# Performance work log

Measured on AMD Instinct MI355X. Metric: run time of the kernel, lower is better.

The kernel has to match this reference:

```python
import jax, jax.numpy as jnp
import numpy as np

L, B, D = 1024, 128, 256  # max_seq_len, batch (dialogues), modality feature dim


def _lin_init(key, shape, fan_in):
    s = 1.0 / np.sqrt(fan_in)
    return jax.random.uniform(key, shape, jnp.float32, -s, s)


def setup_inputs() -> dict:
    key = jax.random.key(0)
    ks = jax.random.split(key, 12)
    inp = {
        'a': jax.random.normal(ks[0], (L, B, D), jnp.float32),
        'v': jax.random.normal(ks[1], (L, B, D), jnp.float32),
        'l': jax.random.normal(ks[2], (L, B, D), jnp.float32),
        # all dialogues padded to full length -> fixed node count (jit-friendly)
        'lengths': jnp.full((B,), L, dtype=jnp.int32),
        # modality transforms: Linear(mem_dim, cand_dim)
        'Wa': _lin_init(ks[3], (D, D), D), 'ba': jnp.zeros((D,), jnp.float32),
        'Wv': _lin_init(ks[4], (D, D), D), 'bv': jnp.zeros((D,), jnp.float32),
        'Wl': _lin_init(ks[5], (D, D), D), 'bl': jnp.zeros((D,), jnp.float32),
        # pairwise gates: Linear(3*mem_dim, 1)
        'Wav': _lin_init(ks[6], (1, 3 * D), 3 * D), 'bav': jnp.zeros((1,), jnp.float32),
        'Wal': _lin_init(ks[7], (1, 3 * D), 3 * D), 'bal': jnp.zeros((1,), jnp.float32),
        'Wvl': _lin_init(ks[8], (1, 3 * D), 3 * D), 'bvl': jnp.zeros((1,), jnp.float32),
    }
    return inp


def _graphify(x, lengths):
    # simple_batch_graphify: cat_j x[:lengths[j], j, :].  With lengths == L this is
    # exactly the batch-major flattening of the padded tensor (node order preserved).
    return jnp.transpose(x, (1, 0, 2)).reshape(-1, x.shape[-1])  # (B*L, D)


def reference(a, v, l, lengths, Wa, ba, Wv, bv, Wl, bl, Wav, bav, Wal, bal, Wvl, bvl):
    na = _graphify(a, lengths)  # (N, D)
    nv = _graphify(v, lengths)
    nl = _graphify(l, lengths)

    # MMGatedAttention, att_type='general', modals='avl' (dropout = eval identity)
    ha = jnp.tanh(na @ Wa.T + ba)
    hv = jnp.tanh(nv @ Wv.T + bv)
    hl = jnp.tanh(nl @ Wl.T + bl)

    z_av = jax.nn.sigmoid(jnp.concatenate([na, nv, na * nv], axis=-1) @ Wav.T + bav)  # (N,1)
    h_av = z_av * ha + (1.0 - z_av) * hv

    z_al = jax.nn.sigmoid(jnp.concatenate([na, nl, na * nl], axis=-1) @ Wal.T + bal)
    h_al = z_al * ha + (1.0 - z_al) * hl

    z_vl = jax.nn.sigmoid(jnp.concatenate([nv, nl, nv * nl], axis=-1) @ Wvl.T + bvl)
    h_vl = z_vl * hv + (1.0 - z_vl) * hl

    return jnp.concatenate([h_av, h_al, h_vl], axis=-1)  # (N, 3D)
```

## Files before the change

kernel.cpp:

```cpp
#include <hip/hip_runtime.h>
#include <hip/hip_bf16.h>

#define L_SEQ 1024
#define B_DLG 128
#define D_DIM 256
#define BM 32
#define THREADS 512
#define KSTEPS 8
#define NTILES (L_SEQ / BM)

typedef __attribute__((ext_vector_type(8))) short short8;
typedef __attribute__((ext_vector_type(4))) float f32x4;

__device__ __forceinline__ float bfbits_to_f(unsigned short u) {
    return __uint_as_float(((unsigned int)u) << 16);
}
__device__ __forceinline__ unsigned short f_to_bfbits(float f) {
    unsigned int u = __float_as_uint(f);
    unsigned int r = (u + 0x7FFFu + ((u >> 16) & 1u)) >> 16;
    return (unsigned short)r;
}
__device__ __forceinline__ float fast_tanh(float x) {
    return 1.0f - 2.0f / (__expf(2.0f * x) + 1.0f);
}
__device__ __forceinline__ float fast_sigmoid(float x) {
    return 1.0f / (1.0f + __expf(-x));
}
__device__ __forceinline__ float dot4(float4 x, float4 w) {
    return x.x * w.x + x.y * w.y + x.z * w.z + x.w * w.w;
}

__global__ void wconv_kernel(const float* __restrict__ wa,
                             const float* __restrict__ wv,
                             const float* __restrict__ wl,
                             unsigned short* __restrict__ wb) {
    int i = blockIdx.x * blockDim.x + threadIdx.x;
    int mod  = i >> 13;
    int r    = i & 8191;
    int col  = r >> 5;
    int ks   = (r >> 2) & 7;
    int kblk = r & 3;
    const float* src = (mod == 0) ? wa : (mod == 1) ? wv : wl;
    const float4* s = (const float4*)(src + col * 256 + ks * 32 + kblk * 8);
    float4 lo = s[0], hi = s[1];
    short8 pk;
    pk[0] = (short)f_to_bfbits(lo.x); pk[1] = (short)f_to_bfbits(lo.y);
    pk[2] = (short)f_to_bfbits(lo.z); pk[3] = (short)f_to_bfbits(lo.w);
    pk[4] = (short)f_to_bfbits(hi.x); pk[5] = (short)f_to_bfbits(hi.y);
    pk[6] = (short)f_to_bfbits(hi.z); pk[7] = (short)f_to_bfbits(hi.w);
    int dst = mod * 8192 + (((col >> 4) * 8 + ks) << 6) + kblk * 16 + (col & 15);
    *(short8*)(wb + dst * 8) = pk;
}

__global__ __launch_bounds__(THREADS, 4)
void fused_kernel(const float* __restrict__ a,
                  const float* __restrict__ v,
                  const float* __restrict__ l,
                  const unsigned short* __restrict__ wbf,
                  const float* __restrict__ ba,
                  const float* __restrict__ bv,
                  const float* __restrict__ bl,
                  const float* __restrict__ wav, const float* __restrict__ bav,
                  const float* __restrict__ wal, const float* __restrict__ bal,
                  const float* __restrict__ wvl, const float* __restrict__ bvl,
                  float* __restrict__ out) {
    __shared__ __align__(16) unsigned short lds_a[3][BM][D_DIM];
    __shared__ float lds_z[3][BM];

    const int tid  = threadIdx.x;
    const int wave = tid >> 6;
    const int lane = tid & 63;
    const int bidx = blockIdx.x;
    const int b    = bidx >> 5;
    const int t0   = (bidx & (NTILES - 1)) * BM;

    float4 fa[4], fv[4], fl[4];
#pragma unroll
    for (int i = 0; i < BM / 8; ++i) {
        const int row = wave + 8 * i;
        const size_t gbase = ((size_t)(t0 + row) * B_DLG + b) * D_DIM + lane * 4;
        fa[i] = *(const float4*)(a + gbase);
        fv[i] = *(const float4*)(v + gbase);
        fl[i] = *(const float4*)(l + gbase);
    }

    const int k0 = lane * 4;
    float4 gav0 = *(const float4*)(wav + k0);
    float4 gav1 = *(const float4*)(wav + 256 + k0);
    float4 gav2 = *(const float4*)(wav + 512 + k0);
    float4 gal0 = *(const float4*)(wal + k0);
    float4 gal1 = *(const float4*)(wal + 256 + k0);
    float4 gal2 = *(const float4*)(wal + 512 + k0);
    float4 gvl0 = *(const float4*)(wvl + k0);
    float4 gvl1 = *(const float4*)(wvl + 256 + k0);
    float4 gvl2 = *(const float4*)(wvl + 512 + k0);

    {
        const int swz = (wave & 7) << 4;
        const int boff = (lane * 8) ^ swz;
#pragma unroll
        for (int i = 0; i < BM / 8; ++i) {
            const int row = wave + 8 * i;
            ushort4 pa, pv, pl;
            pa.x = f_to_bfbits(fa[i].x); pa.y = f_to_bfbits(fa[i].y);
            pa.z = f_to_bfbits(fa[i].z); pa.w = f_to_bfbits(fa[i].w);
            pv.x = f_to_bfbits(fv[i].x); pv.y = f_to_bfbits(fv[i].y);
            pv.z = f_to_bfbits(fv[i].z); pv.w = f_to_bfbits(fv[i].w);
            pl.x = f_to_bfbits(fl[i].x); pl.y = f_to_bfbits(fl[i].y);
            pl.z = f_to_bfbits(fl[i].z); pl.w = f_to_bfbits(fl[i].w);
            *(ushort4*)((char*)&lds_a[0][row][0] + boff) = pa;
            *(ushort4*)((char*)&lds_a[1][row][0] + boff) = pv;
            *(ushort4*)((char*)&lds_a[2][row][0] + boff) = pl;

            float4 pav, pal, pvl;
            pav.x = fa[i].x * fv[i].x; pav.y = fa[i].y * fv[i].y;
            pav.z = fa[i].z * fv[i].z; pav.w = fa[i].w * fv[i].w;
            pal.x = fa[i].x * fl[i].x; pal.y = fa[i].y * fl[i].y;
            pal.z = fa[i].z * fl[i].z; pal.w = fa[i].w * fl[i].w;
            pvl.x = fv[i].x * fl[i].x; pvl.y = fv[i].y * fl[i].y;
            pvl.z = fv[i].z * fl[i].z; pvl.w = fv[i].w * fl[i].w;
            float s_av = dot4(fa[i], gav0) + dot4(fv[i], gav1) + dot4(pav, gav2);
            float s_al = dot4(fa[i], gal0) + dot4(fl[i], gal1) + dot4(pal, gal2);
            float s_vl = dot4(fv[i], gvl0) + dot4(fl[i], gvl1) + dot4(pvl, gvl2);

#pragma unroll
            for (int off = 1; off < 64; off <<= 1) {
                s_av += __shfl_xor(s_av, off);
                s_al += __shfl_xor(s_al, off);
                s_vl += __shfl_xor(s_vl, off);
            }
            if (lane == 0) {
                lds_z[0][row] = fast_sigmoid(s_av + bav[0]);
                lds_z[1][row] = fast_sigmoid(s_al + bal[0]);
                lds_z[2][row] = fast_sigmoid(s_vl + bvl[0]);
            }
        }
    }
    __syncthreads();

    f32x4 acc[3][2][2];
#pragma unroll
    for (int m = 0; m < 3; ++m)
#pragma unroll
        for (int mt = 0; mt < 2; ++mt)
#pragma unroll
            for (int ct = 0; ct < 2; ++ct)
                acc[m][mt][ct] = (f32x4){0.f, 0.f, 0.f, 0.f};

    const int l15 = lane & 15;
    const int kblk = lane >> 4;

#pragma unroll 2
    for (int ks = 0; ks < KSTEPS; ++ks) {
        int kbyte = ks * 64 + kblk * 16;
#pragma unroll
        for (int mod = 0; mod < 3; ++mod) {
            short8 afrag[2];
#pragma unroll
            for (int mt = 0; mt < 2; ++mt) {
                int row = mt * 16 + l15;
                int bo = kbyte ^ ((row & 7) << 4);
                afrag[mt] = *(const short8*)((const char*)&lds_a[mod][row][0] + bo);
            }
#pragma unroll
            for (int ct = 0; ct < 2; ++ct) {
                const unsigned short* bp = wbf +
                    ((size_t)(((mod * 16 + wave * 2 + ct) * 8 + ks) * 64) + lane) * 8;
                short8 bfrag = *(const short8*)bp;
#pragma unroll
                for (int mt = 0; mt < 2; ++mt)
                    acc[mod][mt][ct] = __builtin_amdgcn_mfma_f32_16x16x32_bf16(
                        afrag[mt], bfrag, acc[mod][mt][ct], 0, 0, 0);
            }
        }
    }

    __syncthreads();

    const size_t rowbase = (size_t)b * L_SEQ + t0;
    const int colbase = wave * 32;
#pragma unroll
    for (int mt = 0; mt < 2; ++mt) {
#pragma unroll
        for (int ct = 0; ct < 2; ++ct) {
            int col = colbase + ct * 16 + l15;
            float bba = ba[col], bbv = bv[col], bbl = bl[col];
#pragma unroll
            for (int r = 0; r < 4; ++r) {
                int rl_ = mt * 16 + (lane >> 4) * 4 + r;
                float ta = fast_tanh(acc[0][mt][ct][r] + bba);
                float tv = fast_tanh(acc[1][mt][ct][r] + bbv);
                float tl = fast_tanh(acc[2][mt][ct][r] + bbl);
                float zav = lds_z[0][rl_];
                float zal = lds_z[1][rl_];
                float zvl = lds_z[2][rl_];
                float* orow = out + (rowbase + rl_) * (3 * D_DIM);
                orow[col]             = zav * ta + (1.f - zav) * tv;
                orow[D_DIM + col]     = zal * ta + (1.f - zal) * tl;
                orow[2 * D_DIM + col] = zvl * tv + (1.f - zvl) * tl;
            }
        }
    }
}

extern "C" void kernel_launch(void* const* d_in, const int* in_sizes, int n_in,
                              void* d_out, int out_size, void* d_ws, size_t ws_size,
                              hipStream_t stream) {
    const float* a   = (const float*)d_in[0];
    const float* v   = (const float*)d_in[1];
    const float* l   = (const float*)d_in[2];
    const float* Wa  = (const float*)d_in[4];
    const float* ba  = (const float*)d_in[5];
    const float* Wv  = (const float*)d_in[6];
    const float* bv  = (const float*)d_in[7];
    const float* Wl  = (const float*)d_in[8];
    const float* bl  = (const float*)d_in[9];
    const float* Wav = (const float*)d_in[10];
    const float* bav = (const float*)d_in[11];
    const float* Wal = (const float*)d_in[12];
    const float* bal = (const float*)d_in[13];
    const float* Wvl = (const float*)d_in[14];
    const float* bvl = (const float*)d_in[15];
    float* out = (float*)d_out;

    unsigned short* wb = (unsigned short*)d_ws;

    hipLaunchKernelGGL(wconv_kernel, dim3(96), dim3(256), 0, stream, Wa, Wv, Wl, wb);
    hipLaunchKernelGGL(fused_kernel, dim3(B_DLG * NTILES), dim3(THREADS), 0, stream,
                       a, v, l, wb, ba, bv, bl, Wav, bav, Wal, bal, Wvl, bvl, out);
}
```

Measured before the change: 282.6 us.

## Make fused kernel persistent over eight row tiles with register prefetch of next tile

Each block now handles eight consecutive 32-row tiles of one dialogue instead of one, which cuts the grid from 4096 to 512 blocks. Gate weights are staged once into LDS and bias values are hoisted out of the loop. The next tile's a/v/l rows are loaded into registers before the MFMA and epilogue of the current tile, so global-load latency overlaps with compute. In exchange there are fewer blocks to spread across CUs (512 blocks of 512 threads), a serial per-block loop, and extra LDS plus register pressure.

```diff
diff --git a/kernel.cpp b/kernel.cpp
--- a/kernel.cpp
+++ b/kernel.cpp
@@ -7,14 +7,12 @@
 #define BM 32
 #define THREADS 512
 #define KSTEPS 8
-#define NTILES (L_SEQ / BM)
+#define TPB 8
+#define NBLK (B_DLG * (L_SEQ / BM) / TPB)
 
 typedef __attribute__((ext_vector_type(8))) short short8;
 typedef __attribute__((ext_vector_type(4))) float f32x4;
 
-__device__ __forceinline__ float bfbits_to_f(unsigned short u) {
-    return __uint_as_float(((unsigned int)u) << 16);
-}
 __device__ __forceinline__ unsigned short f_to_bfbits(float f) {
     unsigned int u = __float_as_uint(f);
     unsigned int r = (u + 0x7FFFu + ((u >> 16) & 1u)) >> 16;
@@ -65,139 +63,170 @@
                   const float* __restrict__ wvl, const float* __restrict__ bvl,
                   float* __restrict__ out) {
     __shared__ __align__(16) unsigned short lds_a[3][BM][D_DIM];
+    __shared__ __align__(16) float lds_gw[3][3 * D_DIM];
     __shared__ float lds_z[3][BM];
 
     const int tid  = threadIdx.x;
     const int wave = tid >> 6;
     const int lane = tid & 63;
-    const int bidx = blockIdx.x;
-    const int b    = bidx >> 5;
-    const int t0   = (bidx & (NTILES - 1)) * BM;
-
-    float4 fa[4], fv[4], fl[4];
-#pragma unroll
-    for (int i = 0; i < BM / 8; ++i) {
-        const int row = wave + 8 * i;
-        const size_t gbase = ((size_t)(t0 + row) * B_DLG + b) * D_DIM + lane * 4;
-        fa[i] = *(const float4*)(a + gbase);
-        fv[i] = *(const float4*)(v + gbase);
-        fl[i] = *(const float4*)(l + gbase);
+    const int b    = blockIdx.x >> 2;
+    const int t00  = (blockIdx.x & 3) * (TPB * BM);
+
+    for (int i = tid; i < 3 * 3 * D_DIM; i += THREADS) {
+        int g = i / (3 * D_DIM);
+        int k = i - g * (3 * D_DIM);
+        const float* gw = (g == 0) ? wav : (g == 1) ? wal : wvl;
+        lds_gw[g][k] = gw[k];
     }
-
-    const int k0 = lane * 4;
-    float4 gav0 = *(const float4*)(wav + k0);
-    float4 gav1 = *(const float4*)(wav + 256 + k0);
-    float4 gav2 = *(const float4*)(wav + 512 + k0);
-    float4 gal0 = *(const float4*)(wal + k0);
-    float4 gal1 = *(const float4*)(wal + 256 + k0);
-    float4 gal2 = *(const float4*)(wal + 512 + k0);
-    float4 gvl0 = *(const float4*)(wvl + k0);
-    float4 gvl1 = *(const float4*)(wvl + 256 + k0);
-    float4 gvl2 = *(const float4*)(wvl + 512 + k0);
-
-    {
-        const int swz = (wave & 7) << 4;
-        const int boff = (lane * 8) ^ swz;
-#pragma unroll
-        for (int i = 0; i < BM / 8; ++i) {
-            const int row = wave + 8 * i;
-            ushort4 pa, pv, pl;
-            pa.x = f_to_bfbits(fa[i].x); pa.y = f_to_bfbits(fa[i].y);
-            pa.z = f_to_bfbits(fa[i].z); pa.w = f_to_bfbits(fa[i].w);
-            pv.x = f_to_bfbits(fv[i].x); pv.y = f_to_bfbits(fv[i].y);
-            pv.z = f_to_bfbits(fv[i].z); pv.w = f_to_bfbits(fv[i].w);
-            pl.x = f_to_bfbits(fl[i].x); pl.y = f_to_bfbits(fl[i].y);
-            pl.z = f_to_bfbits(fl[i].z); pl.w = f_to_bfbits(fl[i].w);
-            *(ushort4*)((char*)&lds_a[0][row][0] + boff) = pa;
-            *(ushort4*)((char*)&lds_a[1][row][0] + boff) = pv;
-            *(ushort4*)((char*)&lds_a[2][row][0] + boff) = pl;
-
-            float4 pav, pal, pvl;
-            pav.x = fa[i].x * fv[i].x; pav.y = fa[i].y * fv[i].y;
-            pav.z = fa[i].z * fv[i].z; pav.w = fa[i].w * fv[i].w;
-            pal.x = fa[i].x * fl[i].x; pal.y = fa[i].y * fl[i].y;
-            pal.z = fa[i].z * fl[i].z; pal.w = fa[i].w * fl[i].w;
-            pvl.x = fv[i].x * fl[i].x; pvl.y = fv[i].y * fl[i].y;
-            pvl.z = fv[i].z * fl[i].z; pvl.w = fv[i].w * fl[i].w;
-            float s_av = dot4(fa[i], gav0) + dot4(fv[i], gav1) + dot4(pav, gav2);
-            float s_al = dot4(fa[i], gal0) + dot4(fl[i], gal1) + dot4(pal, gal2);
-            float s_vl = dot4(fv[i], gvl0) + dot4(fl[i], gvl1) + dot4(pvl, gvl2);
-
-#pragma unroll
-            for (int off = 1; off < 64; off <<= 1) {
-                s_av += __shfl_xor(s_av, off);
-                s_al += __shfl_xor(s_al, off);
-                s_vl += __shfl_xor(s_vl, off);
-            }
-            if (lane == 0) {
-                lds_z[0][row] = fast_sigmoid(s_av + bav[0]);
-                lds_z[1][row] = fast_sigmoid(s_al + bal[0]);
-                lds_z[2][row] = fast_sigmoid(s_vl + bvl[0]);
-            }
-        }
-    }
-    __syncthreads();
-
-    f32x4 acc[3][2][2];
-#pragma unroll
-    for (int m = 0; m < 3; ++m)
-#pragma unroll
-        for (int mt = 0; mt < 2; ++mt)
-#pragma unroll
-            for (int ct = 0; ct < 2; ++ct)
-                acc[m][mt][ct] = (f32x4){0.f, 0.f, 0.f, 0.f};
-
     const int l15 = lane & 15;
     const int kblk = lane >> 4;
+    const int colbase = wave * 32;
+    const int col0 = colbase + l15, col1 = colbase + 16 + l15;
+    const float bba0 = ba[col0], bba1 = ba[col1];
+    const float bbv0 = bv[col0], bbv1 = bv[col1];
+    const float bbl0 = bl[col0], bbl1 = bl[col1];
+    const float gbav = bav[0], gbal = bal[0], gbvl = bvl[0];
+
+    float4 fa[4], fv[4], fl[4];
+    {
+        const int t0 = t00;
+#pragma unroll
+        for (int i = 0; i < 4; ++i) {
+            const int row = wave + 8 * i;
+            const size_t gbase = ((size_t)(t0 + row) * B_DLG + b) * D_DIM + lane * 4;
+            fa[i] = *(const float4*)(a + gbase);
+            fv[i] = *(const float4*)(v + gbase);
+            fl[i] = *(const float4*)(l + gbase);
+        }
+    }
+
+    const int swz = (wave & 7) << 4;
+    const int boff = (lane * 8) ^ swz;
+    const int k0 = lane * 4;
+
+#pragma unroll 1
+    for (int it = 0; it < TPB; ++it) {
+        const int t0 = t00 + it * BM;
+        __syncthreads();
+
+        {
+            float4 gav0 = *(const float4*)&lds_gw[0][k0];
+            float4 gav1 = *(const float4*)&lds_gw[0][256 + k0];
+            float4 gav2 = *(const float4*)&lds_gw[0][512 + k0];
+            float4 gal0 = *(const float4*)&lds_gw[1][k0];
+            float4 gal1 = *(const float4*)&lds_gw[1][256 + k0];
+            float4 gal2 = *(const float4*)&lds_gw[1][512 + k0];
+            float4 gvl0 = *(const float4*)&lds_gw[2][k0];
+            float4 gvl1 = *(const float4*)&lds_gw[2][256 + k0];
+            float4 gvl2 = *(const float4*)&lds_gw[2][512 + k0];
+#pragma unroll
+            for (int i = 0; i < 4; ++i) {
+                const int row = wave + 8 * i;
+                ushort4 pa, pv, pl;
+                pa.x = f_to_bfbits(fa[i].x); pa.y = f_to_bfbits(fa[i].y);
+                pa.z = f_to_bfbits(fa[i].z); pa.w = f_to_bfbits(fa[i].w);
+                pv.x = f_to_bfbits(fv[i].x); pv.y = f_to_bfbits(fv[i].y);
+                pv.z = f_to_bfbits(fv[i].z); pv.w = f_to_bfbits(fv[i].w);
+                pl.x = f_to_bfbits(fl[i].x); pl.y = f_to_bfbits(fl[i].y);
+                pl.z = f_to_bfbits(fl[i].z); pl.w = f_to_bfbits(fl[i].w);
+                *(ushort4*)((char*)&lds_a[0][row][0] + boff) = pa;
+                *(ushort4*)((char*)&lds_a[1][row][0] + boff) = pv;
+                *(ushort4*)((char*)&lds_a[2][row][0] + boff) = pl;
+
+                float4 pav, pal, pvl;
+                pav.x = fa[i].x * fv[i].x; pav.y = fa[i].y * fv[i].y;
+                pav.z = fa[i].z * fv[i].z; pav.w = fa[i].w * fv[i].w;
+                pal.x = fa[i].x * fl[i].x; pal.y = fa[i].y * fl[i].y;
+                pal.z = fa[i].z * fl[i].z; pal.w = fa[i].w * fl[i].w;
+                pvl.x = fv[i].x * fl[i].x; pvl.y = fv[i].y * fl[i].y;
+                pvl.z = fv[i].z * fl[i].z; pvl.w = fv[i].w * fl[i].w;
+                float s_av = dot4(fa[i], gav0) + dot4(fv[i], gav1) + dot4(pav, gav2);
+                float s_al = dot4(fa[i], gal0) + dot4(fl[i], gal1) + dot4(pal, gal2);
+                float s_vl = dot4(fv[i], gvl0) + dot4(fl[i], gvl1) + dot4(pvl, gvl2);
+#pragma unroll
+                for (int off = 1; off < 64; off <<= 1) {
+                    s_av += __shfl_xor(s_av, off);
+                    s_al += __shfl_xor(s_al, off);
+                    s_vl += __shfl_xor(s_vl, off);
+                }
+                if (lane == 0) {
+                    lds_z[0][row] = fast_sigmoid(s_av + gbav);
+                    lds_z[1][row] = fast_sigmoid(s_al + gbal);
+                    lds_z[2][row] = fast_sigmoid(s_vl + gbvl);
+                }
+            }
+        }
+        __syncthreads();
+
+        if (it + 1 < TPB) {
+            const int nt0 = t0 + BM;
+#pragma unroll
+            for (int i = 0; i < 4; ++i) {
+                const int row = wave + 8 * i;
+                const size_t gbase = ((size_t)(nt0 + row) * B_DLG + b) * D_DIM + lane * 4;
+                fa[i] = *(const float4*)(a + gbase);
+                fv[i] = *(const float4*)(v + gbase);
+                fl[i] = *(const float4*)(l + gbase);
+            }
+        }
+
+        f32x4 acc[3][2][2];
+#pragma unroll
+        for (int m = 0; m < 3; ++m)
+#pragma unroll
+            for (int mt = 0; mt < 2; ++mt)
+#pragma unroll
+                for (int ct = 0; ct < 2; ++ct)
+                    acc[m][mt][ct] = (f32x4){0.f, 0.f, 0.f, 0.f};
 
 #pragma unroll 2
-    for (int ks = 0; ks < KSTEPS; ++ks) {
-        int kbyte = ks * 64 + kblk * 16;
-#pragma unroll
-        for (int mod = 0; mod < 3; ++mod) {
-            short8 afrag[2];
-#pragma unroll
-            for (int mt = 0; mt < 2; ++mt) {
-                int row = mt * 16 + l15;
-                int bo = kbyte ^ ((row & 7) << 4);
-                afrag[mt] = *(const short8*)((const char*)&lds_a[mod][row][0] + bo);
-            }
+        for (int ks = 0; ks < KSTEPS; ++ks) {
+            int kbyte = ks * 64 + kblk * 16;
+#pragma unroll
+            for (int mod = 0; mod < 3; ++mod) {
+                short8 afrag[2];
+#pragma unroll
+                for (int mt = 0; mt < 2; ++mt) {
+                    int row = mt * 16 + l15;
+                    int bo = kbyte ^ ((row & 7) << 4);
+                    afrag[mt] = *(const short8*)((const char*)&lds_a[mod][row][0] + bo);
+                }
+#pragma unroll
+                for (int ct = 0; ct < 2; ++ct) {
+                    const unsigned short* bp = wbf +
+                        ((size_t)(((mod * 16 + wave * 2 + ct) * 8 + ks) * 64) + lane) * 8;
+                    short8 bfrag = *(const short8*)bp;
+#pragma unroll
+                    for (int mt = 0; mt < 2; ++mt)
+                        acc[mod][mt][ct] = __builtin_amdgcn_mfma_f32_16x16x32_bf16(
+                            afrag[mt], bfrag, acc[mod][mt][ct], 0, 0, 0);
+                }
+            }
+        }
+
+        const size_t rowbase = (size_t)b * L_SEQ + t0;
+#pragma unroll
+        for (int mt = 0; mt < 2; ++mt) {
 #pragma unroll
             for (int ct = 0; ct < 2; ++ct) {
-                const unsigned short* bp = wbf +
-                    ((size_t)(((mod * 16 + wave * 2 + ct) * 8 + ks) * 64) + lane) * 8;
-                short8 bfrag = *(const short8*)bp;
-#pragma unroll
-                for (int mt = 0; mt < 2; ++mt)
-                    acc[mod][mt][ct] = __builtin_amdgcn_mfma_f32_16x16x32_bf16(
-                        afrag[mt], bfrag, acc[mod][mt][ct], 0, 0, 0);
-            }
-        }
-    }
-
-    __syncthreads();
-
-    const size_t rowbase = (size_t)b * L_SEQ + t0;
-    const int colbase = wave * 32;
-#pragma unroll
-    for (int mt = 0; mt < 2; ++mt) {
-#pragma unroll
-        for (int ct = 0; ct < 2; ++ct) {
-            int col = colbase + ct * 16 + l15;
-            float bba = ba[col], bbv = bv[col], bbl = bl[col];
-#pragma unroll
-            for (int r = 0; r < 4; ++r) {
-                int rl_ = mt * 16 + (lane >> 4) * 4 + r;
-                float ta = fast_tanh(acc[0][mt][ct][r] + bba);
-                float tv = fast_tanh(acc[1][mt][ct][r] + bbv);
-                float tl = fast_tanh(acc[2][mt][ct][r] + bbl);
-                float zav = lds_z[0][rl_];
-                float zal = lds_z[1][rl_];
-                float zvl = lds_z[2][rl_];
-                float* orow = out + (rowbase + rl_) * (3 * D_DIM);
-                orow[col]             = zav * ta + (1.f - zav) * tv;
-                orow[D_DIM + col]     = zal * ta + (1.f - zal) * tl;
-                orow[2 * D_DIM + col] = zvl * tv + (1.f - zvl) * tl;
+                const int col = (ct == 0) ? col0 : col1;
+                const float bba = (ct == 0) ? bba0 : bba1;
+                const float bbv = (ct == 0) ? bbv0 : bbv1;
+                const float bbl = (ct == 0) ? bbl0 : bbl1;
+#pragma unroll
+                for (int r = 0; r < 4; ++r) {
+                    int rl_ = mt * 16 + kblk * 4 + r;
+                    float ta = fast_tanh(acc[0][mt][ct][r] + bba);
+                    float tv = fast_tanh(acc[1][mt][ct][r] + bbv);
+                    float tl = fast_tanh(acc[2][mt][ct][r] + bbl);
+                    float zav = lds_z[0][rl_];
+                    float zal = lds_z[1][rl_];
+                    float zvl = lds_z[2][rl_];
+                    float* orow = out + (rowbase + rl_) * (3 * D_DIM);
+                    orow[col]             = zav * ta + (1.f - zav) * tv;
+                    orow[D_DIM + col]     = zal * ta + (1.f - zal) * tl;
+                    orow[2 * D_DIM + col] = zvl * tv + (1.f - zvl) * tl;
+                }
             }
         }
     }
@@ -226,6 +255,6 @@
     unsigned short* wb = (unsigned short*)d_ws;
 
     hipLaunchKernelGGL(wconv_kernel, dim3(96), dim3(256), 0, stream, Wa, Wv, Wl, wb);
-    hipLaunchKernelGGL(fused_kernel, dim3(B_DLG * NTILES), dim3(THREADS), 0, stream,
+    hipLaunchKernelGGL(fused_kernel, dim3(NBLK), dim3(THREADS), 0, stream,
                        a, v, l, wb, ba, bv, bl, Wav, bav, Wal, bal, Wvl, bvl, out);
 }
```

Result: slower. 352.1 us (+24.6%).

## Warp-specialize fused kernel into producer/consumer waves with double-buffered tiles

Applied to the files above, without the earlier changes.

Makes each block persistent over 8 consecutive 16-row tiles. Four producer waves load and convert inputs and compute the gate values into a double-buffered LDS stage. Four consumer waves run the MFMA GEMMs and gating on the previous buffer. Outputs are staged through padded LDS so each global store is a coalesced float4 row write. This is meant to overlap input loading with compute and improve store coalescing, at the cost of fewer blocks, more LDS and producer/consumer barrier coupling.

```diff
diff --git a/kernel.cpp b/kernel.cpp
--- a/kernel.cpp
+++ b/kernel.cpp
@@ -4,17 +4,16 @@
 #define L_SEQ 1024
 #define B_DLG 128
 #define D_DIM 256
-#define BM 32
+#define BM 16
 #define THREADS 512
 #define KSTEPS 8
-#define NTILES (L_SEQ / BM)
+#define TPB 8
+#define NBLK (B_DLG * (L_SEQ / BM) / TPB)
+#define OBROW 68
 
 typedef __attribute__((ext_vector_type(8))) short short8;
 typedef __attribute__((ext_vector_type(4))) float f32x4;
 
-__device__ __forceinline__ float bfbits_to_f(unsigned short u) {
-    return __uint_as_float(((unsigned int)u) << 16);
-}
 __device__ __forceinline__ unsigned short f_to_bfbits(float f) {
     unsigned int u = __float_as_uint(f);
     unsigned int r = (u + 0x7FFFu + ((u >> 16) & 1u)) >> 16;
@@ -28,6 +27,12 @@
 }
 __device__ __forceinline__ float dot4(float4 x, float4 w) {
     return x.x * w.x + x.y * w.y + x.z * w.z + x.w * w.w;
+}
+
+__device__ __forceinline__ void lds_barrier() {
+    asm volatile("s_waitcnt lgkmcnt(0)" ::: "memory");
+    __builtin_amdgcn_s_barrier();
+    __builtin_amdgcn_sched_barrier(0);
 }
 
 __global__ void wconv_kernel(const float* __restrict__ wa,
@@ -64,141 +69,168 @@
                   const float* __restrict__ wal, const float* __restrict__ bal,
                   const float* __restrict__ wvl, const float* __restrict__ bvl,
                   float* __restrict__ out) {
-    __shared__ __align__(16) unsigned short lds_a[3][BM][D_DIM];
-    __shared__ float lds_z[3][BM];
+    __shared__ __align__(16) unsigned short lds_a[2][3][BM][D_DIM];
+    __shared__ float lds_z[2][3][BM];
+    __shared__ __align__(16) float lds_ob[4][BM * OBROW];
 
     const int tid  = threadIdx.x;
     const int wave = tid >> 6;
     const int lane = tid & 63;
-    const int bidx = blockIdx.x;
-    const int b    = bidx >> 5;
-    const int t0   = (bidx & (NTILES - 1)) * BM;
-
-    float4 fa[4], fv[4], fl[4];
-#pragma unroll
-    for (int i = 0; i < BM / 8; ++i) {
-        const int row = wave + 8 * i;
-        const size_t gbase = ((size_t)(t0 + row) * B_DLG + b) * D_DIM + lane * 4;
-        fa[i] = *(const float4*)(a + gbase);
-        fv[i] = *(const float4*)(v + gbase);
-        fl[i] = *(const float4*)(l + gbase);
-    }
-
-    const int k0 = lane * 4;
-    float4 gav0 = *(const float4*)(wav + k0);
-    float4 gav1 = *(const float4*)(wav + 256 + k0);
-    float4 gav2 = *(const float4*)(wav + 512 + k0);
-    float4 gal0 = *(const float4*)(wal + k0);
-    float4 gal1 = *(const float4*)(wal + 256 + k0);
-    float4 gal2 = *(const float4*)(wal + 512 + k0);
-    float4 gvl0 = *(const float4*)(wvl + k0);
-    float4 gvl1 = *(const float4*)(wvl + 256 + k0);
-    float4 gvl2 = *(const float4*)(wvl + 512 + k0);
-
-    {
-        const int swz = (wave & 7) << 4;
-        const int boff = (lane * 8) ^ swz;
-#pragma unroll
-        for (int i = 0; i < BM / 8; ++i) {
-            const int row = wave + 8 * i;
-            ushort4 pa, pv, pl;
-            pa.x = f_to_bfbits(fa[i].x); pa.y = f_to_bfbits(fa[i].y);
-            pa.z = f_to_bfbits(fa[i].z); pa.w = f_to_bfbits(fa[i].w);
-            pv.x = f_to_bfbits(fv[i].x); pv.y = f_to_bfbits(fv[i].y);
-            pv.z = f_to_bfbits(fv[i].z); pv.w = f_to_bfbits(fv[i].w);
-            pl.x = f_to_bfbits(fl[i].x); pl.y = f_to_bfbits(fl[i].y);
-            pl.z = f_to_bfbits(fl[i].z); pl.w = f_to_bfbits(fl[i].w);
-            *(ushort4*)((char*)&lds_a[0][row][0] + boff) = pa;
-            *(ushort4*)((char*)&lds_a[1][row][0] + boff) = pv;
-            *(ushort4*)((char*)&lds_a[2][row][0] + boff) = pl;
-
-            float4 pav, pal, pvl;
-            pav.x = fa[i].x * fv[i].x; pav.y = fa[i].y * fv[i].y;
-            pav.z = fa[i].z * fv[i].z; pav.w = fa[i].w * fv[i].w;
-            pal.x = fa[i].x * fl[i].x; pal.y = fa[i].y * fl[i].y;
-            pal.z = fa[i].z * fl[i].z; pal.w = fa[i].w * fl[i].w;
-            pvl.x = fv[i].x * fl[i].x; pvl.y = fv[i].y * fl[i].y;
-            pvl.z = fv[i].z * fl[i].z; pvl.w = fv[i].w * fl[i].w;
-            float s_av = dot4(fa[i], gav0) + dot4(fv[i], gav1) + dot4(pav, gav2);
-            float s_al = dot4(fa[i], gal0) + dot4(fl[i], gal1) + dot4(pal, gal2);
-            float s_vl = dot4(fv[i], gvl0) + dot4(fl[i], gvl1) + dot4(pvl, gvl2);
-
-#pragma unroll
-            for (int off = 1; off < 64; off <<= 1) {
-                s_av += __shfl_xor(s_av, off);
-                s_al += __shfl_xor(s_al, off);
-                s_vl += __shfl_xor(s_vl, off);
-            }
-            if (lane == 0) {
-                lds_z[0][row] = fast_sigmoid(s_av + bav[0]);
-                lds_z[1][row] = fast_sigmoid(s_al + bal[0]);
-                lds_z[2][row] = fast_sigmoid(s_vl + bvl[0]);
-            }
+    const int b    = blockIdx.x >> 3;
+    const int t00  = (blockIdx.x & 7) * (TPB * BM);
+
+    if (wave < 4) {
+        const int k0 = lane * 4;
+        float4 gav0 = *(const float4*)(wav + k0);
+        float4 gav1 = *(const float4*)(wav + 256 + k0);
+        float4 gav2 = *(const float4*)(wav + 512 + k0);
+        float4 gal0 = *(const float4*)(wal + k0);
+        float4 gal1 = *(const float4*)(wal + 256 + k0);
+        float4 gal2 = *(const float4*)(wal + 512 + k0);
+        float4 gvl0 = *(const float4*)(wvl + k0);
+        float4 gvl1 = *(const float4*)(wvl + 256 + k0);
+        float4 gvl2 = *(const float4*)(wvl + 512 + k0);
+        const float gbav = bav[0], gbal = bal[0], gbvl = bvl[0];
+
+        auto stage = [&](int t0, int buf) {
+            float4 fa[4], fv[4], fl[4];
+#pragma unroll
+            for (int i = 0; i < 4; ++i) {
+                const int row = wave * 4 + i;
+                const size_t gbase = ((size_t)(t0 + row) * B_DLG + b) * D_DIM + lane * 4;
+                fa[i] = *(const float4*)(a + gbase);
+                fv[i] = *(const float4*)(v + gbase);
+                fl[i] = *(const float4*)(l + gbase);
+            }
+#pragma unroll
+            for (int i = 0; i < 4; ++i) {
+                const int row = wave * 4 + i;
+                const int boff = (lane * 8) ^ ((row & 7) << 4);
+                ushort4 pa, pv, pl;
+                pa.x = f_to_bfbits(fa[i].x); pa.y = f_to_bfbits(fa[i].y);
+                pa.z = f_to_bfbits(fa[i].z); pa.w = f_to_bfbits(fa[i].w);
+                pv.x = f_to_bfbits(fv[i].x); pv.y = f_to_bfbits(fv[i].y);
+                pv.z = f_to_bfbits(fv[i].z); pv.w = f_to_bfbits(fv[i].w);
+                pl.x = f_to_bfbits(fl[i].x); pl.y = f_to_bfbits(fl[i].y);
+                pl.z = f_to_bfbits(fl[i].z); pl.w = f_to_bfbits(fl[i].w);
+                *(ushort4*)((char*)&lds_a[buf][0][row][0] + boff) = pa;
+                *(ushort4*)((char*)&lds_a[buf][1][row][0] + boff) = pv;
+                *(ushort4*)((char*)&lds_a[buf][2][row][0] + boff) = pl;
+
+                float4 pav, pal, pvl;
+                pav.x = fa[i].x * fv[i].x; pav.y = fa[i].y * fv[i].y;
+                pav.z = fa[i].z * fv[i].z; pav.w = fa[i].w * fv[i].w;
+                pal.x = fa[i].x * fl[i].x; pal.y = fa[i].y * fl[i].y;
+                pal.z = fa[i].z * fl[i].z; pal.w = fa[i].w * fl[i].w;
+                pvl.x = fv[i].x * fl[i].x; pvl.y = fv[i].y * fl[i].y;
+                pvl.z = fv[i].z * fl[i].z; pvl.w = fv[i].w * fl[i].w;
+                float s_av = dot4(fa[i], gav0) + dot4(fv[i], gav1) + dot4(pav, gav2);
+                float s_al = dot4(fa[i], gal0) + dot4(fl[i], gal1) + dot4(pal, gal2);
+                float s_vl = dot4(fv[i], gvl0) + dot4(fl[i], gvl1) + dot4(pvl, gvl2);
+#pragma unroll
+                for (int off = 1; off < 64; off <<= 1) {
+                    s_av += __shfl_xor(s_av, off);
+                    s_al += __shfl_xor(s_al, off);
+                    s_vl += __shfl_xor(s_vl, off);
+                }
+                if (lane == 0) {
+                    lds_z[buf][0][row] = fast_sigmoid(s_av + gbav);
+                    lds_z[buf][1][row] = fast_sigmoid(s_al + gbal);
+                    lds_z[buf][2][row] = fast_sigmoid(s_vl + gbvl);
+                }
+            }
+        };
+
+        stage(t00, 0);
+        lds_barrier();
+#pragma unroll 1
+        for (int t = 0; t < TPB; ++t) {
+            if (t + 1 < TPB) stage(t00 + (t + 1) * BM, (t + 1) & 1);
+            lds_barrier();
         }
-    }
-    __syncthreads();
-
-    f32x4 acc[3][2][2];
-#pragma unroll
-    for (int m = 0; m < 3; ++m)
-#pragma unroll
-        for (int mt = 0; mt < 2; ++mt)
-#pragma unroll
-            for (int ct = 0; ct < 2; ++ct)
-                acc[m][mt][ct] = (f32x4){0.f, 0.f, 0.f, 0.f};
-
-    const int l15 = lane & 15;
-    const int kblk = lane >> 4;
+    } else {
+        const int cw   = wave - 4;
+        const int l15  = lane & 15;
+        const int kblk = lane >> 4;
+        float bba[4], bbv[4], bbl[4];
+#pragma unroll
+        for (int ct = 0; ct < 4; ++ct) {
+            const int col = cw * 64 + ct * 16 + l15;
+            bba[ct] = ba[col]; bbv[ct] = bv[col]; bbl[ct] = bl[col];
+        }
+        float* ob = lds_ob[cw];
+
+        lds_barrier();
+#pragma unroll 1
+        for (int t = 0; t < TPB; ++t) {
+            const int t0  = t00 + t * BM;
+            const int buf = t & 1;
+
+            f32x4 acc[3][4];
+#pragma unroll
+            for (int m = 0; m < 3; ++m)
+#pragma unroll
+                for (int ct = 0; ct < 4; ++ct)
+                    acc[m][ct] = (f32x4){0.f, 0.f, 0.f, 0.f};
 
 #pragma unroll 2
-    for (int ks = 0; ks < KSTEPS; ++ks) {
-        int kbyte = ks * 64 + kblk * 16;
-#pragma unroll
-        for (int mod = 0; mod < 3; ++mod) {
-            short8 afrag[2];
-#pragma unroll
-            for (int mt = 0; mt < 2; ++mt) {
-                int row = mt * 16 + l15;
-                int bo = kbyte ^ ((row & 7) << 4);
-                afrag[mt] = *(const short8*)((const char*)&lds_a[mod][row][0] + bo);
-            }
-#pragma unroll
-            for (int ct = 0; ct < 2; ++ct) {
-                const unsigned short* bp = wbf +
-                    ((size_t)(((mod * 16 + wave * 2 + ct) * 8 + ks) * 64) + lane) * 8;
-                short8 bfrag = *(const short8*)bp;
-#pragma unroll
-                for (int mt = 0; mt < 2; ++mt)
-                    acc[mod][mt][ct] = __builtin_amdgcn_mfma_f32_16x16x32_bf16(
-                        afrag[mt], bfrag, acc[mod][mt][ct], 0, 0, 0);
-            }
-        }
-    }
-
-    __syncthreads();
-
-    const size_t rowbase = (size_t)b * L_SEQ + t0;
-    const int colbase = wave * 32;
-#pragma unroll
-    for (int mt = 0; mt < 2; ++mt) {
-#pragma unroll
-        for (int ct = 0; ct < 2; ++ct) {
-            int col = colbase + ct * 16 + l15;
-            float bba = ba[col], bbv = bv[col], bbl = bl[col];
-#pragma unroll
-            for (int r = 0; r < 4; ++r) {
-                int rl_ = mt * 16 + (lane >> 4) * 4 + r;
-                float ta = fast_tanh(acc[0][mt][ct][r] + bba);
-                float tv = fast_tanh(acc[1][mt][ct][r] + bbv);
-                float tl = fast_tanh(acc[2][mt][ct][r] + bbl);
-                float zav = lds_z[0][rl_];
-                float zal = lds_z[1][rl_];
-                float zvl = lds_z[2][rl_];
-                float* orow = out + (rowbase + rl_) * (3 * D_DIM);
-                orow[col]             = zav * ta + (1.f - zav) * tv;
-                orow[D_DIM + col]     = zal * ta + (1.f - zal) * tl;
-                orow[2 * D_DIM + col] = zvl * tv + (1.f - zvl) * tl;
-            }
+            for (int ks = 0; ks < KSTEPS; ++ks) {
+                int kbyte = ks * 64 + kblk * 16;
+#pragma unroll
+                for (int mod = 0; mod < 3; ++mod) {
+                    int bo = kbyte ^ ((l15 & 7) << 4);
+                    short8 afrag = *(const short8*)
+                        ((const char*)&lds_a[buf][mod][l15][0] + bo);
+#pragma unroll
+                    for (int ct = 0; ct < 4; ++ct) {
+                        const unsigned short* bp = wbf +
+                            ((size_t)(((mod * 16 + cw * 4 + ct) * 8 + ks) * 64) + lane) * 8;
+                        short8 bfrag = *(const short8*)bp;
+                        acc[mod][ct] = __builtin_amdgcn_mfma_f32_16x16x32_bf16(
+                            afrag, bfrag, acc[mod][ct], 0, 0, 0);
+                    }
+                }
+            }
+
+#pragma unroll
+            for (int ct = 0; ct < 4; ++ct)
+#pragma unroll
+                for (int r = 0; r < 4; ++r) {
+                    acc[0][ct][r] = fast_tanh(acc[0][ct][r] + bba[ct]);
+                    acc[1][ct][r] = fast_tanh(acc[1][ct][r] + bbv[ct]);
+                    acc[2][ct][r] = fast_tanh(acc[2][ct][r] + bbl[ct]);
+                }
+
+            const size_t rowbase = (size_t)b * L_SEQ + t0;
+#pragma unroll
+            for (int sec = 0; sec < 3; ++sec) {
+                const int mA = (sec == 2) ? 1 : 0;
+                const int mB = (sec == 0) ? 1 : 2;
+#pragma unroll
+                for (int ct = 0; ct < 4; ++ct)
+#pragma unroll
+                    for (int r = 0; r < 4; ++r) {
+                        const int row = kblk * 4 + r;
+                        const float h1 = acc[mA][ct][r];
+                        const float h2 = acc[mB][ct][r];
+                        const float z  = lds_z[buf][sec][row];
+                        ob[row * OBROW + ct * 16 + l15] = h2 + z * (h1 - h2);
+                    }
+                asm volatile("s_waitcnt lgkmcnt(0)" ::: "memory");
+                __builtin_amdgcn_sched_barrier(0);
+#pragma unroll
+                for (int q = 0; q < 2; ++q) {
+#pragma unroll
+                    for (int ch = 0; ch < 2; ++ch) {
+                        const int rt   = q * 8 + (lane >> 3);
+                        const int colq = lane & 7;
+                        float4 val = *(const float4*)&ob[rt * OBROW + ch * 32 + colq * 4];
+                        *(float4*)(out + (rowbase + rt) * (3 * D_DIM)
+                                       + sec * D_DIM + cw * 64 + ch * 32 + colq * 4) = val;
+                    }
+                }
+            }
+            lds_barrier();
         }
     }
 }
@@ -226,6 +258,6 @@
     unsigned short* wb = (unsigned short*)d_ws;
 
     hipLaunchKernelGGL(wconv_kernel, dim3(96), dim3(256), 0, stream, Wa, Wv, Wl, wb);
-    hipLaunchKernelGGL(fused_kernel, dim3(B_DLG * NTILES), dim3(THREADS), 0, stream,
+    hipLaunchKernelGGL(fused_kernel, dim3(NBLK), dim3(THREADS), 0, stream,
                        a, v, l, wb, ba, bv, bl, Wav, bav, Wal, bal, Wvl, bvl, out);
 }
```

Measured after the change: 478.6 us. +69.4%, slower.
